# Kernel optimization log

Hardware: AMD Instinct MI355X
Metric: run time of the kernel (lower is better)

## Reference

```python
import jax, jax.numpy as jnp
import numpy as np

B, E, F, H, C = 2048, 16, 512, 1024, 512
TOP_K = 4
TEMP = 1.0


def setup_inputs() -> dict:
    key = jax.random.key(0)
    ks = jax.random.split(key, 5)
    h = jax.random.normal(ks[0], (B, F), jnp.float32)
    # Router posterior params (xavier-ish mu, logvar init at -7 as in torch code)
    W_mu = jax.random.normal(ks[1], (E, F), jnp.float32) * (1.0 / np.sqrt(F))
    W_logvar = jnp.full((E, F), -7.0, jnp.float32)
    b_mu = jnp.zeros((E,), jnp.float32)
    b_logvar = jnp.full((E,), -7.0, jnp.float32)
    # Expert MLP params: layer1 [F->H] relu, layer2 [H->C]
    W1 = jax.random.normal(ks[2], (E, F, H), jnp.float32) * (1.0 / np.sqrt(F))
    b1 = jnp.zeros((E, H), jnp.float32)
    W2 = jax.random.normal(ks[3], (E, H, C), jnp.float32) * (1.0 / np.sqrt(H))
    b2 = jnp.zeros((E, C), jnp.float32)
    return {"h": h, "W_mu": W_mu, "b_mu": b_mu, "W_logvar": W_logvar,
            "b_logvar": b_logvar, "W1": W1, "b1": b1, "W2": W2, "b2": b2}


def reference(h, W_mu, b_mu, W_logvar, b_logvar, W1, b1, W2, b2):
    # Bayesian router moments: mu = h @ W_mu^T + b_mu ; var = (h*h) @ exp(W_logvar)^T + exp(b_logvar)
    mu_m = h @ W_mu.T + b_mu                                   # [B,E]
    var_m = (h * h) @ jnp.exp(W_logvar).T + jnp.exp(b_logvar)  # [B,E]
    var_m = jnp.maximum(var_m, 1e-12)
    # Logistic-normal shrink: tilde = mu / sqrt(1 + (pi/8) var)
    tilde_m = mu_m / jnp.sqrt(1.0 + (jnp.pi / 8.0) * var_m)
    gate_probs = jax.nn.softmax(tilde_m / TEMP, axis=-1)       # [B,E]
    # Strict top-k by gate_scores (tilde_m), renormalize probs within top-k
    topk_scores, topk_idx = jax.lax.top_k(tilde_m, TOP_K)      # [B,k]
    topk_w = jnp.take_along_axis(gate_probs, topk_idx, axis=1) # [B,k]
    topk_w = topk_w / jnp.maximum(topk_w.sum(axis=1, keepdims=True), 1e-12)
    # Dense combine weights: w[b,e] = sum of renormalized top-k weights of token b for expert e
    Bsz = h.shape[0]
    w = jnp.zeros((Bsz, E), h.dtype).at[jnp.arange(Bsz)[:, None], topk_idx].add(topk_w)
    # Expert MLPs (grouped GEMM form); tokens not routed to expert e get weight 0
    a = jax.nn.relu(jnp.einsum('bf,efh->beh', h, W1) + b1)     # [B,E,H]
    y = jnp.einsum('beh,ehc->bec', a, W2) + b2                 # [B,E,C]
    combined = jnp.einsum('be,bec->bc', w, y)                  # [B,C]
    return combined
```

## Files before the change

kernel.cpp:

```cpp
#include <hip/hip_runtime.h>
#include <hip/hip_bf16.h>

typedef __attribute__((ext_vector_type(8))) short bf16x8;
typedef __attribute__((ext_vector_type(4))) float f32x4;

#define NTOK   2048
#define NEXP   16
#define NF     512
#define NH     1024
#define NCOUT  512
#define NPAIR  8192

__device__ __forceinline__ void gload16_lds(const __hip_bfloat16* g, const __hip_bfloat16* l) {
  __builtin_amdgcn_global_load_lds((const __attribute__((address_space(1))) void*)g,
                                   (__attribute__((address_space(3))) void*)l, 16, 0, 0);
}

__global__ __launch_bounds__(256) void prep_kernel(
    const float* __restrict__ h, const float* __restrict__ W_mu,
    const float* __restrict__ b_mu, const float* __restrict__ W_logvar,
    const float* __restrict__ b_logvar,
    int* __restrict__ topk_idx, float* __restrict__ topk_w,
    __hip_bfloat16* __restrict__ hb,
    const float* __restrict__ W1, __hip_bfloat16* __restrict__ W1t,
    const float* __restrict__ W2, __hip_bfloat16* __restrict__ W2t)
{
  __shared__ float smem[64 * 33];
  __shared__ float smu[NEXP], svar[NEXP];
  const int tid = threadIdx.x;

  if (blockIdx.x < NTOK) {
    float* hs  = smem;
    float* hs2 = smem + NF;
    const int b = blockIdx.x;
    for (int i = tid; i < NF; i += 256) {
      float v = h[(size_t)b * NF + i];
      hs[i] = v; hs2[i] = v * v;
      hb[(size_t)b * NF + i] = __float2bfloat16(v);
    }
    __syncthreads();
    const int e = tid >> 4, l = tid & 15;
    float mu = 0.f, var = 0.f;
    const float4* wm4 = (const float4*)(W_mu + e * NF);
    const float4* wv4 = (const float4*)(W_logvar + e * NF);
    const float4* h4  = (const float4*)hs;
    const float4* h24 = (const float4*)hs2;
#pragma unroll
    for (int j = 0; j < NF / 64; ++j) {
      int i4 = l + j * 16;
      float4 a = h4[i4],  wa = wm4[i4];
      float4 c = h24[i4], wc = wv4[i4];
      mu  += a.x * wa.x + a.y * wa.y + a.z * wa.z + a.w * wa.w;
      var += c.x * __expf(wc.x) + c.y * __expf(wc.y) + c.z * __expf(wc.z) + c.w * __expf(wc.w);
    }
#pragma unroll
    for (int o = 1; o < 16; o <<= 1) { mu += __shfl_xor(mu, o); var += __shfl_xor(var, o); }
    if (l == 0) { smu[e] = mu + b_mu[e]; svar[e] = var + __expf(b_logvar[e]); }
    __syncthreads();
    if (tid < 64) {
      float val = -1e30f;
      if (tid < NEXP) {
        float v = fmaxf(svar[tid], 1e-12f);
        val = smu[tid] / sqrtf(1.0f + 0.39269908169872414f * v);
      }
      float mx = 0.f, wsum = 0.f;
      int i0, i1, i2, i3; float p0, p1, p2, p3;
#define TOPK_ROUND(ii, pp, FIRST)                                          \
      {                                                                    \
        float m = val;                                                     \
        m = fmaxf(m, __shfl_xor(m, 1));  m = fmaxf(m, __shfl_xor(m, 2));   \
        m = fmaxf(m, __shfl_xor(m, 4));  m = fmaxf(m, __shfl_xor(m, 8));   \
        m = fmaxf(m, __shfl_xor(m, 16)); m = fmaxf(m, __shfl_xor(m, 32));  \
        unsigned long long bm = __ballot(val == m);                        \
        int bi = (int)__builtin_ctzll(bm);                                 \
        if (FIRST) mx = m;                                                 \
        pp = expf(m - mx); wsum += pp; ii = bi;                            \
        if (tid == bi) val = -1e30f;                                       \
      }
      TOPK_ROUND(i0, p0, 1)
      TOPK_ROUND(i1, p1, 0)
      TOPK_ROUND(i2, p2, 0)
      TOPK_ROUND(i3, p3, 0)
#undef TOPK_ROUND
      if (tid == 0) {
        float inv = 1.0f / fmaxf(wsum, 1e-12f);
        topk_idx[b * 4 + 0] = i0; topk_w[b * 4 + 0] = p0 * inv;
        topk_idx[b * 4 + 1] = i1; topk_w[b * 4 + 1] = p1 * inv;
        topk_idx[b * 4 + 2] = i2; topk_w[b * 4 + 2] = p2 * inv;
        topk_idx[b * 4 + 3] = i3; topk_w[b * 4 + 3] = p3 * inv;
      }
    }
  } else {
    const int bid = blockIdx.x - NTOK;
    const float* in; __hip_bfloat16* out; int R, C, e, cx, ry;
    if (bid < 4096) {
      in = W1; out = W1t; R = NF; C = NH;
      e = bid >> 8; cx = bid & 31; ry = (bid >> 5) & 7;
    } else {
      in = W2; out = W2t; R = NH; C = NCOUT;
      const int b2 = bid - 4096;
      e = b2 >> 8; cx = b2 & 15; ry = (b2 >> 4) & 15;
    }
    float (*tile)[33] = (float (*)[33])smem;
    const int r0 = ry * 64, c0 = cx * 32;
    const int x = tid & 31, y = tid >> 5;
    const float* ip = in + ((size_t)e * R + r0) * C + c0;
#pragma unroll
    for (int i = 0; i < 8; ++i) tile[y + 8 * i][x] = ip[(size_t)(y + 8 * i) * C + x];
    __syncthreads();
    const int rp = tid & 31, cb = tid >> 5;
#pragma unroll
    for (int j = 0; j < 4; ++j) {
      const int c = cb + 8 * j;
      union { __hip_bfloat16 b[2]; unsigned u; } v;
      v.b[0] = __float2bfloat16(tile[2 * rp][c]);
      v.b[1] = __float2bfloat16(tile[2 * rp + 1][c]);
      *(unsigned*)(out + ((size_t)e * C + c0 + c) * R + r0 + 2 * rp) = v.u;
    }
  }
}

__global__ __launch_bounds__(1024) void route_finish_kernel(
    const int* __restrict__ topk_idx,
    int* __restrict__ counts, int* __restrict__ offsets,
    int* __restrict__ token_of_row, int* __restrict__ pair_row)
{
  __shared__ int cnt[128][16];
  __shared__ int choff[128][2];
  __shared__ int tot[16];
  __shared__ int soff[16];
  const int tid = threadIdx.x;
  const int wv = tid >> 6, ln = tid & 63;
  const int e0 = blockIdx.x * 2;
  int mye[8], myrank[8];
#pragma unroll
  for (int r = 0; r < 8; ++r) {
    const int chunk = r * 16 + wv;
    const int t = chunk * 64 + ln;
    const int e = topk_idx[t];
    mye[r] = e;
    unsigned long long mymask = 0;
#pragma unroll
    for (int ee = 0; ee < 16; ++ee) {
      unsigned long long bmask = __ballot(e == ee);
      if (ln == 0) cnt[chunk][ee] = __popcll(bmask);
      if (e == ee) mymask = bmask;
    }
    myrank[r] = __popcll(mymask & ((1ull << ln) - 1ull));
  }
  __syncthreads();
  if (tid < 16) {
    int run = 0;
    for (int c = 0; c < 128; ++c) run += cnt[c][tid];
    tot[tid] = run;
    if (blockIdx.x == 0) counts[tid] = run;
  }
  if (tid >= 32 && tid < 34) {
    const int e = e0 + (tid - 32);
    int run = 0;
    for (int c = 0; c < 128; ++c) { choff[c][tid - 32] = run; run += cnt[c][e]; }
  }
  __syncthreads();
  if (tid == 0) {
    int run = 0;
    for (int e2 = 0; e2 < NEXP; ++e2) {
      soff[e2] = run;
      if (blockIdx.x == 0) offsets[e2] = run;
      run += tot[e2];
    }
  }
  __syncthreads();
#pragma unroll
  for (int r = 0; r < 8; ++r) {
    const int e = mye[r];
    if (e == e0 || e == e0 + 1) {
      const int chunk = r * 16 + wv;
      const int t = chunk * 64 + ln;
      const int pos = soff[e] + choff[chunk][e - e0] + myrank[r];
      token_of_row[pos] = t >> 2;
      pair_row[t] = pos;
    }
  }
}


__global__ __launch_bounds__(256) void gemm1_kernel(
    const __hip_bfloat16* __restrict__ hb,
    const __hip_bfloat16* __restrict__ W1t,
    const float* __restrict__ b1,
    const int* __restrict__ token_of_row, const int* __restrict__ offsets,
    const int* __restrict__ counts,
    __hip_bfloat16* __restrict__ a_out)
{
  const int bid = blockIdx.x;
  const int id  = (bid & 7) * 512 + (bid >> 3);
  const int e   = id >> 8;
  const int m0  = ((id >> 4) & 15) * 128;
  const int n0  = (id & 15) * 64;
  const int cnt = counts[e];
  if (m0 >= cnt) return;
  const int off = offsets[e];

  __shared__ __align__(16) __hip_bfloat16 As[128 * 64];
  __shared__ __align__(16) __hip_bfloat16 Bs[64 * 64];

  const int tid = threadIdx.x;
  const int w = tid >> 6, l = tid & 63;
  const int wm = w >> 1, wn = w & 1;
  const int r16 = l & 15, g4 = l >> 4;
  const int sx = r16 & 7;
  const int koffL = (((l & 7) ^ (l >> 3)) * 8);

  const __hip_bfloat16* Aptr[4];
#pragma unroll
  for (int i = 0; i < 4; ++i) {
    int r = off + m0 + w * 32 + i * 8 + (l >> 3);
    if (r > NPAIR - 1) r = NPAIR - 1;
    Aptr[i] = hb + (size_t)token_of_row[r] * NF + koffL;
  }
  const __hip_bfloat16* Bptr[2];
#pragma unroll
  for (int i = 0; i < 2; ++i)
    Bptr[i] = W1t + ((size_t)e * NH + n0 + w * 16 + i * 8 + (l >> 3)) * NF + koffL;

  f32x4 acc[4][2] = {};

  for (int k0 = 0; k0 < NF; k0 += 64) {
    __syncthreads();
#pragma unroll
    for (int i = 0; i < 4; ++i) gload16_lds(Aptr[i] + k0, As + (w * 32 + i * 8) * 64);
#pragma unroll
    for (int i = 0; i < 2; ++i) gload16_lds(Bptr[i] + k0, Bs + (w * 16 + i * 8) * 64);
    __syncthreads();
#pragma unroll
    for (int ks = 0; ks < 2; ++ks) {
      const int seg = (ks * 4 + g4) ^ sx;
      bf16x8 af[4], bq[2];
#pragma unroll
      for (int rr = 0; rr < 4; ++rr)
        af[rr] = *(const bf16x8*)(As + (wm * 64 + rr * 16 + r16) * 64 + seg * 8);
#pragma unroll
      for (int nn = 0; nn < 2; ++nn)
        bq[nn] = *(const bf16x8*)(Bs + (wn * 32 + nn * 16 + r16) * 64 + seg * 8);
#pragma unroll
      for (int rr = 0; rr < 4; ++rr)
#pragma unroll
        for (int nn = 0; nn < 2; ++nn)
          acc[rr][nn] = __builtin_amdgcn_mfma_f32_16x16x32_bf16(af[rr], bq[nn], acc[rr][nn], 0, 0, 0);
    }
  }

  const int q4 = l >> 4, cl = l & 15;
  const int mmax = cnt - m0;
#pragma unroll
  for (int rr = 0; rr < 4; ++rr) {
#pragma unroll
    for (int nn = 0; nn < 2; ++nn) {
      const int c = n0 + wn * 32 + nn * 16 + cl;
      const float bias = b1[e * NH + c];
#pragma unroll
      for (int q = 0; q < 4; ++q) {
        const int r = wm * 64 + rr * 16 + q4 * 4 + q;
        if (r < mmax) {
          float v = fmaxf(acc[rr][nn][q] + bias, 0.f);
          a_out[(size_t)(off + m0 + r) * NH + c] = __float2bfloat16(v);
        }
      }
    }
  }
}

__global__ __launch_bounds__(256) void gemm2_kernel(
    const __hip_bfloat16* __restrict__ a_in,
    const __hip_bfloat16* __restrict__ W2t,
    const float* __restrict__ b2,
    const int* __restrict__ offsets, const int* __restrict__ counts,
    float* __restrict__ ybuf)
{
  const int bid = blockIdx.x;
  const int id  = (bid & 7) * 256 + (bid >> 3);
  const int e   = id >> 7;
  const int m0  = ((id >> 3) & 15) * 128;
  const int n0  = (id & 7) * 64;
  const int cnt = counts[e];
  if (m0 >= cnt) return;
  const int off = offsets[e];

  __shared__ __align__(16) __hip_bfloat16 As[128 * 64];
  __shared__ __align__(16) __hip_bfloat16 Bs[64 * 64];

  const int tid = threadIdx.x;
  const int w = tid >> 6, l = tid & 63;
  const int wm = w >> 1, wn = w & 1;
  const int r16 = l & 15, g4 = l >> 4;
  const int sx = r16 & 7;
  const int koffL = (((l & 7) ^ (l >> 3)) * 8);

  const __hip_bfloat16* Aptr[4];
#pragma unroll
  for (int i = 0; i < 4; ++i) {
    int r = off + m0 + w * 32 + i * 8 + (l >> 3);
    if (r > NPAIR - 1) r = NPAIR - 1;
    Aptr[i] = a_in + (size_t)r * NH + koffL;
  }
  const __hip_bfloat16* Bptr[2];
#pragma unroll
  for (int i = 0; i < 2; ++i)
    Bptr[i] = W2t + ((size_t)e * NCOUT + n0 + w * 16 + i * 8 + (l >> 3)) * NH + koffL;

  f32x4 acc[4][2] = {};

  for (int k0 = 0; k0 < NH; k0 += 64) {
    __syncthreads();
#pragma unroll
    for (int i = 0; i < 4; ++i) gload16_lds(Aptr[i] + k0, As + (w * 32 + i * 8) * 64);
#pragma unroll
    for (int i = 0; i < 2; ++i) gload16_lds(Bptr[i] + k0, Bs + (w * 16 + i * 8) * 64);
    __syncthreads();
#pragma unroll
    for (int ks = 0; ks < 2; ++ks) {
      const int seg = (ks * 4 + g4) ^ sx;
      bf16x8 af[4], bq[2];
#pragma unroll
      for (int rr = 0; rr < 4; ++rr)
        af[rr] = *(const bf16x8*)(As + (wm * 64 + rr * 16 + r16) * 64 + seg * 8);
#pragma unroll
      for (int nn = 0; nn < 2; ++nn)
        bq[nn] = *(const bf16x8*)(Bs + (wn * 32 + nn * 16 + r16) * 64 + seg * 8);
#pragma unroll
      for (int rr = 0; rr < 4; ++rr)
#pragma unroll
        for (int nn = 0; nn < 2; ++nn)
          acc[rr][nn] = __builtin_amdgcn_mfma_f32_16x16x32_bf16(af[rr], bq[nn], acc[rr][nn], 0, 0, 0);
    }
  }

  const int q4 = l >> 4, cl = l & 15;
  const int mmax = cnt - m0;
#pragma unroll
  for (int rr = 0; rr < 4; ++rr) {
#pragma unroll
    for (int nn = 0; nn < 2; ++nn) {
      const int c = n0 + wn * 32 + nn * 16 + cl;
      const float bias = b2[e * NCOUT + c];
#pragma unroll
      for (int q = 0; q < 4; ++q) {
        const int r = wm * 64 + rr * 16 + q4 * 4 + q;
        if (r < mmax)
          ybuf[(size_t)(off + m0 + r) * NCOUT + c] = acc[rr][nn][q] + bias;
      }
    }
  }
}

__global__ __launch_bounds__(256) void combine_kernel(
    const float* __restrict__ ybuf, const int* __restrict__ pair_row,
    const float* __restrict__ topk_w, float* __restrict__ out)
{
  const int tok = blockIdx.x;
  const int c = threadIdx.x * 2;
  float a0 = 0.f, a1 = 0.f;
#pragma unroll
  for (int k = 0; k < 4; ++k) {
    const int t = tok * 4 + k;
    const float wt = topk_w[t];
    const float2 y = *(const float2*)(ybuf + (size_t)pair_row[t] * NCOUT + c);
    a0 += wt * y.x; a1 += wt * y.y;
  }
  *(float2*)(out + (size_t)tok * NCOUT + c) = make_float2(a0, a1);
}

extern "C" void kernel_launch(void* const* d_in, const int* in_sizes, int n_in,
                              void* d_out, int out_size, void* d_ws, size_t ws_size,
                              hipStream_t stream) {
  (void)in_sizes; (void)n_in; (void)ws_size; (void)out_size;
  const float* h        = (const float*)d_in[0];
  const float* W_mu     = (const float*)d_in[1];
  const float* b_mu     = (const float*)d_in[2];
  const float* W_logvar = (const float*)d_in[3];
  const float* b_logvar = (const float*)d_in[4];
  const float* W1       = (const float*)d_in[5];
  const float* b1       = (const float*)d_in[6];
  const float* W2       = (const float*)d_in[7];
  const float* b2       = (const float*)d_in[8];
  float* out = (float*)d_out;

  char* p = (char*)d_ws;
  int*   counts   = (int*)p;   p += 16 * 4;
  int*   offsets  = (int*)p;   p += 16 * 4;
  p += 32 * 4;
  int*   topk_idx = (int*)p;   p += (size_t)NPAIR * 4;
  float* topk_w   = (float*)p; p += (size_t)NPAIR * 4;
  int*   tok_row  = (int*)p;   p += (size_t)NPAIR * 4;
  int*   pair_row = (int*)p;   p += (size_t)NPAIR * 4;
  __hip_bfloat16* hb   = (__hip_bfloat16*)p; p += (size_t)NTOK * NF * 2;
  __hip_bfloat16* W1t  = (__hip_bfloat16*)p; p += (size_t)NEXP * NF * NH * 2;
  __hip_bfloat16* W2t  = (__hip_bfloat16*)p; p += (size_t)NEXP * NH * NCOUT * 2;
  __hip_bfloat16* abuf = (__hip_bfloat16*)p; p += (size_t)NPAIR * NH * 2;
  float*          ybuf = (float*)p;          p += (size_t)NPAIR * NCOUT * 4;

  prep_kernel<<<NTOK + 8192, 256, 0, stream>>>(h, W_mu, b_mu, W_logvar, b_logvar,
                                               topk_idx, topk_w, hb, W1, W1t, W2, W2t);
  route_finish_kernel<<<8, 1024, 0, stream>>>(topk_idx, counts, offsets, tok_row, pair_row);

  gemm1_kernel<<<4096, 256, 0, stream>>>(hb, W1t, b1, tok_row, offsets, counts, abuf);
  gemm2_kernel<<<2048, 256, 0, stream>>>(abuf, W2t, b2, offsets, counts, ybuf);
  combine_kernel<<<NTOK, 256, 0, stream>>>(ybuf, pair_row, topk_w, out);
}
```

Baseline: 87.10 us.

## Use compact routed panel list for grouped GEMMs and store expert outputs in bf16

The routing kernel now emits a compact list of 128-row panels (expert, start row, row count) so the GEMM grids hold only useful tiles (1280 and 640 blocks instead of 4096 and 2048 mostly-empty ones). This removes launch and early-exit overhead and improves the block-to-CU spread. The second GEMM also writes its output in bf16 and the combine kernel reads bf16, which halves that intermediate traffic at some precision cost. The panel count is capped at 80, so a skewed routing could overflow the list.

```diff
diff --git a/kernel.cpp b/kernel.cpp
--- a/kernel.cpp
+++ b/kernel.cpp
@@ -10,6 +10,7 @@
 #define NH     1024
 #define NCOUT  512
 #define NPAIR  8192
+#define MAXPAN 80
 
 __device__ __forceinline__ void gload16_lds(const __hip_bfloat16* g, const __hip_bfloat16* l) {
   __builtin_amdgcn_global_load_lds((const __attribute__((address_space(1))) void*)g,
@@ -122,8 +123,8 @@
 
 __global__ __launch_bounds__(1024) void route_finish_kernel(
     const int* __restrict__ topk_idx,
-    int* __restrict__ counts, int* __restrict__ offsets,
-    int* __restrict__ token_of_row, int* __restrict__ pair_row)
+    int* __restrict__ token_of_row, int* __restrict__ pair_row,
+    unsigned* __restrict__ pinfo)
 {
   __shared__ int cnt[128][16];
   __shared__ int choff[128][2];
@@ -153,7 +154,6 @@
     int run = 0;
     for (int c = 0; c < 128; ++c) run += cnt[c][tid];
     tot[tid] = run;
-    if (blockIdx.x == 0) counts[tid] = run;
   }
   if (tid >= 32 && tid < 34) {
     const int e = e0 + (tid - 32);
@@ -163,10 +163,17 @@
   __syncthreads();
   if (tid == 0) {
     int run = 0;
-    for (int e2 = 0; e2 < NEXP; ++e2) {
-      soff[e2] = run;
-      if (blockIdx.x == 0) offsets[e2] = run;
-      run += tot[e2];
+    for (int e2 = 0; e2 < NEXP; ++e2) { soff[e2] = run; run += tot[e2]; }
+    if (blockIdx.x == 0) {
+      int np = 0;
+      for (int e2 = 0; e2 < NEXP; ++e2) {
+        for (int r0 = 0; r0 < tot[e2]; r0 += 128) {
+          pinfo[2 * np]     = ((unsigned)e2 << 16) | (unsigned)(soff[e2] + r0);
+          pinfo[2 * np + 1] = (unsigned)((tot[e2] - r0 < 128) ? (tot[e2] - r0) : 128);
+          ++np;
+        }
+      }
+      for (; np < MAXPAN; ++np) pinfo[2 * np] = 0xFFFFFFFFu;
     }
   }
   __syncthreads();
@@ -188,18 +195,19 @@
     const __hip_bfloat16* __restrict__ hb,
     const __hip_bfloat16* __restrict__ W1t,
     const float* __restrict__ b1,
-    const int* __restrict__ token_of_row, const int* __restrict__ offsets,
-    const int* __restrict__ counts,
+    const int* __restrict__ token_of_row,
+    const unsigned* __restrict__ pinfo,
     __hip_bfloat16* __restrict__ a_out)
 {
   const int bid = blockIdx.x;
-  const int id  = (bid & 7) * 512 + (bid >> 3);
-  const int e   = id >> 8;
-  const int m0  = ((id >> 4) & 15) * 128;
-  const int n0  = (id & 15) * 64;
-  const int cnt = counts[e];
-  if (m0 >= cnt) return;
-  const int off = offsets[e];
+  const int id  = (bid & 7) * 160 + (bid >> 3);
+  const int p   = id >> 4;
+  const unsigned pw = pinfo[2 * p];
+  if (pw == 0xFFFFFFFFu) return;
+  const int e    = (int)(pw >> 16);
+  const int row0 = (int)(pw & 0xFFFFu);
+  const int rows = (int)pinfo[2 * p + 1];
+  const int n0   = (id & 15) * 64;
 
   __shared__ __align__(16) __hip_bfloat16 As[128 * 64];
   __shared__ __align__(16) __hip_bfloat16 Bs[64 * 64];
@@ -214,7 +222,7 @@
   const __hip_bfloat16* Aptr[4];
 #pragma unroll
   for (int i = 0; i < 4; ++i) {
-    int r = off + m0 + w * 32 + i * 8 + (l >> 3);
+    int r = row0 + w * 32 + i * 8 + (l >> 3);
     if (r > NPAIR - 1) r = NPAIR - 1;
     Aptr[i] = hb + (size_t)token_of_row[r] * NF + koffL;
   }
@@ -251,7 +259,6 @@
   }
 
   const int q4 = l >> 4, cl = l & 15;
-  const int mmax = cnt - m0;
 #pragma unroll
   for (int rr = 0; rr < 4; ++rr) {
 #pragma unroll
@@ -261,9 +268,9 @@
 #pragma unroll
       for (int q = 0; q < 4; ++q) {
         const int r = wm * 64 + rr * 16 + q4 * 4 + q;
-        if (r < mmax) {
+        if (r < rows) {
           float v = fmaxf(acc[rr][nn][q] + bias, 0.f);
-          a_out[(size_t)(off + m0 + r) * NH + c] = __float2bfloat16(v);
+          a_out[(size_t)(row0 + r) * NH + c] = __float2bfloat16(v);
         }
       }
     }
@@ -274,17 +281,18 @@
     const __hip_bfloat16* __restrict__ a_in,
     const __hip_bfloat16* __restrict__ W2t,
     const float* __restrict__ b2,
-    const int* __restrict__ offsets, const int* __restrict__ counts,
-    float* __restrict__ ybuf)
+    const unsigned* __restrict__ pinfo,
+    __hip_bfloat16* __restrict__ ybuf)
 {
   const int bid = blockIdx.x;
-  const int id  = (bid & 7) * 256 + (bid >> 3);
-  const int e   = id >> 7;
-  const int m0  = ((id >> 3) & 15) * 128;
-  const int n0  = (id & 7) * 64;
-  const int cnt = counts[e];
-  if (m0 >= cnt) return;
-  const int off = offsets[e];
+  const int id  = (bid & 7) * 80 + (bid >> 3);
+  const int p   = id >> 3;
+  const unsigned pw = pinfo[2 * p];
+  if (pw == 0xFFFFFFFFu) return;
+  const int e    = (int)(pw >> 16);
+  const int row0 = (int)(pw & 0xFFFFu);
+  const int rows = (int)pinfo[2 * p + 1];
+  const int n0   = (id & 7) * 64;
 
   __shared__ __align__(16) __hip_bfloat16 As[128 * 64];
   __shared__ __align__(16) __hip_bfloat16 Bs[64 * 64];
@@ -299,7 +307,7 @@
   const __hip_bfloat16* Aptr[4];
 #pragma unroll
   for (int i = 0; i < 4; ++i) {
-    int r = off + m0 + w * 32 + i * 8 + (l >> 3);
+    int r = row0 + w * 32 + i * 8 + (l >> 3);
     if (r > NPAIR - 1) r = NPAIR - 1;
     Aptr[i] = a_in + (size_t)r * NH + koffL;
   }
@@ -336,7 +344,6 @@
   }
 
   const int q4 = l >> 4, cl = l & 15;
-  const int mmax = cnt - m0;
 #pragma unroll
   for (int rr = 0; rr < 4; ++rr) {
 #pragma unroll
@@ -346,15 +353,15 @@
 #pragma unroll
       for (int q = 0; q < 4; ++q) {
         const int r = wm * 64 + rr * 16 + q4 * 4 + q;
-        if (r < mmax)
-          ybuf[(size_t)(off + m0 + r) * NCOUT + c] = acc[rr][nn][q] + bias;
+        if (r < rows)
+          ybuf[(size_t)(row0 + r) * NCOUT + c] = __float2bfloat16(acc[rr][nn][q] + bias);
       }
     }
   }
 }
 
 __global__ __launch_bounds__(256) void combine_kernel(
-    const float* __restrict__ ybuf, const int* __restrict__ pair_row,
+    const __hip_bfloat16* __restrict__ ybuf, const int* __restrict__ pair_row,
     const float* __restrict__ topk_w, float* __restrict__ out)
 {
   const int tok = blockIdx.x;
@@ -364,8 +371,9 @@
   for (int k = 0; k < 4; ++k) {
     const int t = tok * 4 + k;
     const float wt = topk_w[t];
-    const float2 y = *(const float2*)(ybuf + (size_t)pair_row[t] * NCOUT + c);
-    a0 += wt * y.x; a1 += wt * y.y;
+    const unsigned u = *(const unsigned*)(ybuf + (size_t)pair_row[t] * NCOUT + c);
+    a0 += wt * __uint_as_float((u & 0xFFFFu) << 16);
+    a1 += wt * __uint_as_float(u & 0xFFFF0000u);
   }
   *(float2*)(out + (size_t)tok * NCOUT + c) = make_float2(a0, a1);
 }
@@ -386,9 +394,8 @@
   float* out = (float*)d_out;
 
   char* p = (char*)d_ws;
-  int*   counts   = (int*)p;   p += 16 * 4;
-  int*   offsets  = (int*)p;   p += 16 * 4;
-  p += 32 * 4;
+  unsigned* pinfo = (unsigned*)p; p += 2 * MAXPAN * 4;
+  p += 64;
   int*   topk_idx = (int*)p;   p += (size_t)NPAIR * 4;
   float* topk_w   = (float*)p; p += (size_t)NPAIR * 4;
   int*   tok_row  = (int*)p;   p += (size_t)NPAIR * 4;
@@ -397,13 +404,13 @@
   __hip_bfloat16* W1t  = (__hip_bfloat16*)p; p += (size_t)NEXP * NF * NH * 2;
   __hip_bfloat16* W2t  = (__hip_bfloat16*)p; p += (size_t)NEXP * NH * NCOUT * 2;
   __hip_bfloat16* abuf = (__hip_bfloat16*)p; p += (size_t)NPAIR * NH * 2;
-  float*          ybuf = (float*)p;          p += (size_t)NPAIR * NCOUT * 4;
+  __hip_bfloat16* ybuf = (__hip_bfloat16*)p; p += (size_t)NPAIR * NCOUT * 2;
 
   prep_kernel<<<NTOK + 8192, 256, 0, stream>>>(h, W_mu, b_mu, W_logvar, b_logvar,
                                                topk_idx, topk_w, hb, W1, W1t, W2, W2t);
-  route_finish_kernel<<<8, 1024, 0, stream>>>(topk_idx, counts, offsets, tok_row, pair_row);
-
-  gemm1_kernel<<<4096, 256, 0, stream>>>(hb, W1t, b1, tok_row, offsets, counts, abuf);
-  gemm2_kernel<<<2048, 256, 0, stream>>>(abuf, W2t, b2, offsets, counts, ybuf);
+  route_finish_kernel<<<8, 1024, 0, stream>>>(topk_idx, tok_row, pair_row, pinfo);
+
+  gemm1_kernel<<<1280, 256, 0, stream>>>(hb, W1t, b1, tok_row, pinfo, abuf);
+  gemm2_kernel<<<640, 256, 0, stream>>>(abuf, W2t, b2, pinfo, ybuf);
   combine_kernel<<<NTOK, 256, 0, stream>>>(ybuf, pair_row, topk_w, out);
 }
```

Result: slower. 103.5 us (+18.8%).
